# Optimization experiments

Measured on AMD Instinct MI355X. Metric: run time of the kernel, lower is better.

## Reference

```python
import jax, jax.numpy as jnp
import numpy as np

B, S, T, D, H = 2, 2048, 2048, 512, 8
HD = D // H
CLAMP = 1e9


def _padding_cross_mask(key):
    # emulate cross_mask(): valid prefixes for src and tgt sequences
    k1, k2 = jax.random.split(key)
    src_len = jax.random.randint(k1, (B,), S // 2, S + 1)  # [B]
    tgt_len = jax.random.randint(k2, (B,), T // 2, T + 1)  # [B]
    src_valid = jnp.arange(S)[None, :] < src_len[:, None]  # [B,S]
    tgt_valid = jnp.arange(T)[None, :] < tgt_len[:, None]  # [B,T]
    m = tgt_valid[:, :, None] & src_valid[:, None, :]      # [B,T,S]
    return m[:, None, :, :]                                 # [B,1,T,S]


def setup_inputs() -> dict:
    key = jax.random.key(0)
    ks = jax.random.split(key, 10)
    sc = 0.02
    return {
        "x": jax.random.normal(ks[0], (B, S, D), jnp.float32),
        "y": jax.random.normal(ks[1], (B, T, D), jnp.float32),
        "mask": _padding_cross_mask(ks[2]),
        "kv_w": jax.random.normal(ks[3], (D, 2 * D), jnp.float32) * sc,
        "kv_b": jax.random.normal(ks[4], (2 * D,), jnp.float32) * sc,
        "q_w": jax.random.normal(ks[5], (D, D), jnp.float32) * sc,
        "q_b": jax.random.normal(ks[6], (D,), jnp.float32) * sc,
        "o_w": jax.random.normal(ks[7], (D, D), jnp.float32) * sc,
        "o_b": jax.random.normal(ks[8], (D,), jnp.float32) * sc,
    }


def reference(x, y, mask, kv_w, kv_b, q_w, q_b, o_w, o_b):
    b, t, d = y.shape
    s = x.shape[1]
    kv = x @ kv_w + kv_b                               # [B,S,2D]
    q = y @ q_w + q_b                                  # [B,T,D]
    kv = kv.reshape(b, s, H, 2 * HD).transpose(0, 2, 1, 3)  # [B,H,S,2hd]
    q = q.reshape(b, t, H, HD).transpose(0, 2, 1, 3)        # [B,H,T,hd]
    k, v = kv[..., :HD], kv[..., HD:]
    scores = jnp.einsum("bhtd,bhsd->bhts", q, k) / jnp.sqrt(jnp.float32(HD))
    scores = jnp.where(mask, scores, -jnp.inf)
    scores = jnp.clip(scores, -CLAMP, CLAMP)
    attn = jax.nn.softmax(scores, axis=-1)             # [B,H,T,S]
    vals = jnp.einsum("bhts,bhsd->bhtd", attn, v)
    vals = vals.transpose(0, 2, 1, 3).reshape(b, t, d)
    return vals @ o_w + o_b
```

## Files before the change

### kernel.cpp

```cpp
#include <hip/hip_runtime.h>
#include <hip/hip_bf16.h>
#include <stdint.h>

#define BN 2
#define SL 2048
#define TL 2048
#define DD 512
#define HN 8
#define HDIM 64
#define NSPLIT 2
#define NCHUNK ((SL / NSPLIT) / 64)
#define QSCALE 0.1803368801111f
#define MFIX 12.0f

typedef __attribute__((ext_vector_type(8))) short bf16x8;
typedef __attribute__((ext_vector_type(4))) float f32x4;

static __device__ __forceinline__ unsigned short f2bf(float f) {
    union { float f; unsigned int u; } c; c.f = f;
    unsigned int u = c.u;
    unsigned int r = (u + 0x7fffu + ((u >> 16) & 1u)) >> 16;
    return (unsigned short)r;
}

static __device__ __forceinline__ void gload_lds16(const void* g, void* l) {
    __builtin_amdgcn_global_load_lds(
        (const __attribute__((address_space(1))) unsigned int*)g,
        (__attribute__((address_space(3))) unsigned int*)l, 16, 0, 0);
}

__global__ __launch_bounds__(256) void prep_kernel(
    const float* __restrict__ x, const float* __restrict__ y,
    const float* __restrict__ kv_w, const float* __restrict__ q_w,
    const float* __restrict__ o_w, const void* __restrict__ mask,
    unsigned short* __restrict__ xb, unsigned short* __restrict__ yb,
    unsigned short* __restrict__ kvwT, unsigned short* __restrict__ qwT,
    unsigned short* __restrict__ owT, int* __restrict__ lens,
    float* __restrict__ vmean)
{
    __shared__ unsigned short lds[64][80];
    __shared__ int kind_sh;
    __shared__ int lpart[4];
    int bx = blockIdx.x;
    int tid = threadIdx.x;
    if (bx < 2048) {
        const float* src = (bx < 1024) ? x : y;
        unsigned short* dst = (bx < 1024) ? xb : yb;
        long long i = ((long long)(bx & 1023) * 256 + tid) * 8;
        float4 v0 = *(const float4*)&src[i];
        float4 v1 = *(const float4*)&src[i + 4];
        unsigned long long p0 =
            (unsigned long long)f2bf(v0.x) | ((unsigned long long)f2bf(v0.y) << 16) |
            ((unsigned long long)f2bf(v0.z) << 32) | ((unsigned long long)f2bf(v0.w) << 48);
        unsigned long long p1 =
            (unsigned long long)f2bf(v1.x) | ((unsigned long long)f2bf(v1.y) << 16) |
            ((unsigned long long)f2bf(v1.z) << 32) | ((unsigned long long)f2bf(v1.w) << 48);
        *(unsigned long long*)&dst[i] = p0;
        *(unsigned long long*)&dst[i + 4] = p1;
        return;
    }
    if (bx >= 2308) {
        float4 z = {0.f, 0.f, 0.f, 0.f};
        ((float4*)vmean)[tid] = z;
        return;
    }
    if (bx >= 2304) {
        int blk = bx - 2304;
        int b = blk >> 1, is_tgt = blk & 1;
        if (tid == 0) {
            unsigned int v = *(const unsigned int*)mask;
            int kind = 0;
            if (v == 0x01010101u) kind = 1;
            else if (v == 0x3f800000u) kind = 2;
            else if (v == 0x3f803f80u) kind = 3;
            kind_sh = kind;
        }
        __syncthreads();
        int kind = kind_sh;
        int lane = tid & 63, wid = tid >> 6;
        int cnt = 0;
        for (int i = tid; i < (is_tgt ? TL : SL); i += 256) {
            long long idx = is_tgt ? ((long long)(b * TL + i)) * SL
                                   : ((long long)(b * TL + 0)) * SL + i;
            bool bit;
            if (kind == 0)      bit = ((const int*)mask)[idx] != 0;
            else if (kind == 1) bit = ((const unsigned char*)mask)[idx] != 0;
            else if (kind == 2) bit = ((const float*)mask)[idx] != 0.0f;
            else                bit = ((const unsigned short*)mask)[idx] != 0;
            cnt += bit ? 1 : 0;
        }
        #pragma unroll
        for (int off = 32; off >= 1; off >>= 1) cnt += __shfl_xor(cnt, off, 64);
        if (lane == 0) lpart[wid] = cnt;
        __syncthreads();
        if (tid == 0)
            lens[is_tgt * 2 + b] = lpart[0] + lpart[1] + lpart[2] + lpart[3];
        return;
    }
    const float* W; unsigned short* Wt; int N, tb;
    if (bx < 2176)      { W = kv_w; Wt = kvwT; N = 1024; tb = bx - 2048; }
    else if (bx < 2240) { W = q_w;  Wt = qwT;  N = 512;  tb = bx - 2176; }
    else                { W = o_w;  Wt = owT;  N = 512;  tb = bx - 2240; }
    int nblk = N / 64;
    int n0 = (tb % nblk) * 64, k0 = (tb / nblk) * 64;
    #pragma unroll
    for (int i = 0; i < 4; ++i) {
        int fi = tid + i * 256;
        int kl = fi >> 4;
        int nl = (fi & 15) * 4;
        float4 v = *(const float4*)&W[(long long)(k0 + kl) * N + n0 + nl];
        lds[nl + 0][kl] = f2bf(v.x);
        lds[nl + 1][kl] = f2bf(v.y);
        lds[nl + 2][kl] = f2bf(v.z);
        lds[nl + 3][kl] = f2bf(v.w);
    }
    __syncthreads();
    #pragma unroll
    for (int i = 0; i < 2; ++i) {
        int fi = tid + i * 256;
        int nl = fi >> 3;
        int kl = (fi & 7) * 8;
        *(bf16x8*)&Wt[(long long)(n0 + nl) * 512 + k0 + kl] = *(const bf16x8*)&lds[nl][kl];
    }
}

static __device__ __forceinline__ void mainloop_64x128(
    const unsigned short* __restrict__ Ab, const unsigned short* __restrict__ Bt,
    int m0, int n0, int tid,
    unsigned short* Alds,
    unsigned short* Blds,
    f32x4 (&acc)[2][4])
{
    int lane = tid & 63, wid = tid >> 6;
    int wr = wid >> 1, wc = wid & 1;
    int lr = lane & 15, lg = lane >> 4;
    int rl = lane >> 2;
    int sc = (lane & 3) ^ ((rl >> 1) & 3);

    auto stage = [&](int buf, int kt) {
        #pragma unroll
        for (int j = 0; j < 3; ++j) {
            int seg = wid * 3 + j;
            if (seg < 4) {
                int row = seg * 16 + rl;
                gload_lds16(&Ab[((long long)(m0 + row)) * 512 + kt * 32 + sc * 8],
                            (char*)(Alds + buf * 2048) + seg * 1024);
            } else {
                int s2 = seg - 4;
                int row = s2 * 16 + rl;
                gload_lds16(&Bt[((long long)(n0 + row)) * 512 + kt * 32 + sc * 8],
                            (char*)(Blds + buf * 4096) + s2 * 1024);
            }
        }
    };
    auto frag = [&](const unsigned short* base, int row) -> bf16x8 {
        int slot = lg ^ ((row >> 1) & 3);
        return *(const bf16x8*)((const char*)base + row * 64 + slot * 16);
    };

    stage(0, 0);
    stage(1, 1);
    for (int kt = 0; kt < 16; ++kt) {
        int buf = kt & 3;
        if (kt < 15) asm volatile("s_waitcnt vmcnt(3)" ::: "memory");
        else         asm volatile("s_waitcnt vmcnt(0)" ::: "memory");
        __builtin_amdgcn_s_barrier();
        __builtin_amdgcn_sched_barrier(0);
        if (kt + 2 < 16) stage((kt + 2) & 3, kt + 2);
        bf16x8 bfr[4];
        #pragma unroll
        for (int ni = 0; ni < 4; ++ni)
            bfr[ni] = frag(Blds + buf * 4096, wc * 64 + ni * 16 + lr);
        #pragma unroll
        for (int mi = 0; mi < 2; ++mi) {
            bf16x8 afr = frag(Alds + buf * 2048, wr * 32 + mi * 16 + lr);
            #pragma unroll
            for (int ni = 0; ni < 4; ++ni)
                acc[mi][ni] = __builtin_amdgcn_mfma_f32_16x16x32_bf16(
                                  afr, bfr[ni], acc[mi][ni], 0, 0, 0);
        }
    }
}

__global__ __launch_bounds__(256) void gemm_kvq(
    const unsigned short* __restrict__ xb, const unsigned short* __restrict__ yb,
    const unsigned short* __restrict__ kvwT, const unsigned short* __restrict__ qwT,
    const float* __restrict__ kv_b, const float* __restrict__ q_b,
    const int* __restrict__ lens,
    unsigned short* __restrict__ Kbuf, unsigned short* __restrict__ Vtbuf,
    unsigned short* __restrict__ Qbuf, float* __restrict__ vmean)
{
    __shared__ __align__(16) unsigned short Alds[4][64 * 32];
    __shared__ __align__(16) unsigned short Blds[4][128 * 32];
    int gid = blockIdx.x;
    int swz = (gid & 7) * 96 + (gid >> 3);
    int nidx = swz % 12;
    int m0 = (swz / 12) * 64;
    bool isq = nidx >= 8;
    if (isq && (m0 & 2047) >= lens[2 + (m0 >> 11)]) return;
    const unsigned short* Ab = isq ? yb : xb;
    const unsigned short* Bt = isq ? qwT : kvwT;
    const float* bias = isq ? q_b : kv_b;
    int n0 = (isq ? (nidx - 8) : nidx) * 128;
    int tid = threadIdx.x;
    int lane = tid & 63, wid = tid >> 6;
    int wr = wid >> 1, wc = wid & 1;
    int lr = lane & 15, lg = lane >> 4;

    f32x4 acc[2][4] = {};
    mainloop_64x128(Ab, Bt, m0, n0, tid, &Alds[0][0], &Blds[0][0], acc);

    float vsum[4] = {0.f, 0.f, 0.f, 0.f};
    #pragma unroll
    for (int mi = 0; mi < 2; ++mi)
    #pragma unroll
    for (int ni = 0; ni < 4; ++ni) {
        int n = n0 + wc * 64 + ni * 16 + lr;
        int mbase = m0 + wr * 32 + mi * 16 + lg * 4;
        float bv = bias[n];
        int b = mbase >> 11;
        int s = mbase & 2047;
        if (!isq) {
            int h = n >> 7, j = n & 127;
            if (j < HDIM) {
                long long base = (((long long)(b * HN + h)) * SL + s) * HDIM + j;
                #pragma unroll
                for (int r = 0; r < 4; ++r)
                    Kbuf[base + (long long)r * HDIM] = f2bf(acc[mi][ni][r] + bv);
            } else {
                int d = j - HDIM;
                long long base = (((long long)(b * HN + h)) * HDIM + d) * SL + s;
                unsigned long long p = 0;
                #pragma unroll
                for (int r = 0; r < 4; ++r)
                    p |= (unsigned long long)f2bf(acc[mi][ni][r] + bv) << (16 * r);
                *(unsigned long long*)&Vtbuf[base] = p;
                vsum[ni] += ((acc[mi][ni][0] + bv) + (acc[mi][ni][1] + bv)) +
                            ((acc[mi][ni][2] + bv) + (acc[mi][ni][3] + bv));
            }
        } else {
            int h = n >> 6, j = n & 63;
            long long base = (((long long)(b * HN + h)) * TL + s) * HDIM + j;
            #pragma unroll
            for (int r = 0; r < 4; ++r)
                Qbuf[base + (long long)r * HDIM] = f2bf((acc[mi][ni][r] + bv) * QSCALE);
        }
    }
    if (!isq && wc == 1) {
        int bh = (m0 >> 11) * HN + (n0 >> 7);
        #pragma unroll
        for (int ni = 0; ni < 4; ++ni) {
            float v = vsum[ni];
            v += __shfl_xor(v, 16, 64);
            v += __shfl_xor(v, 32, 64);
            if (lg == 0)
                atomicAdd(&vmean[bh * HDIM + ni * 16 + lr], v * (1.0f / SL));
        }
    }
}

__global__ __launch_bounds__(256) void gemm_out(
    const unsigned short* __restrict__ Ab, const unsigned short* __restrict__ Bt,
    const float* __restrict__ bias, float* __restrict__ outF)
{
    __shared__ __align__(16) unsigned short Alds[4][64 * 32];
    __shared__ __align__(16) unsigned short Blds[4][128 * 32];
    const int N = 512;
    int n0 = blockIdx.x * 128;
    int m0 = blockIdx.y * 64;
    int tid = threadIdx.x;
    int lane = tid & 63, wid = tid >> 6;
    int wr = wid >> 1, wc = wid & 1;
    int lr = lane & 15, lg = lane >> 4;

    f32x4 acc[2][4] = {};
    mainloop_64x128(Ab, Bt, m0, n0, tid, &Alds[0][0], &Blds[0][0], acc);

    #pragma unroll
    for (int mi = 0; mi < 2; ++mi)
    #pragma unroll
    for (int ni = 0; ni < 4; ++ni) {
        int n = n0 + wc * 64 + ni * 16 + lr;
        int mbase = m0 + wr * 32 + mi * 16 + lg * 4;
        float bv = bias[n];
        #pragma unroll
        for (int r = 0; r < 4; ++r)
            outF[(long long)(mbase + r) * N + n] = acc[mi][ni][r] + bv;
    }
}

__global__ __launch_bounds__(512) void attn_kernel(
    const unsigned short* __restrict__ Q,
    const unsigned short* __restrict__ K,
    const unsigned short* __restrict__ Vt,
    const int* __restrict__ lens,
    float* __restrict__ pml,
    float* __restrict__ pacc)
{
    __shared__ unsigned short Kt[2][4096];
    __shared__ unsigned short Vl[2][4096];
    __shared__ unsigned int P32[8][16][32];
    int idx = blockIdx.x;
    int gid = (idx & 7) * 64 + (idx >> 3);
    int t0 = (gid & 15) * 128;
    int bhsp = gid >> 4;
    int bh = bhsp >> 1;
    int sp = bhsp & 1;
    int b = bh >> 3;
    int tid = threadIdx.x;
    int lane = tid & 63, wid = tid >> 6;
    int tcol = lane & 15, lg = lane >> 4;
    int t0w = t0 + wid * 16;
    int src_len = lens[b];
    int tgt_len = lens[2 + b];
    if (t0 >= tgt_len) return;
    int sbase = sp * (SL / NSPLIT);

    int nch = (src_len - sbase + 63) >> 6;
    if (nch > NCHUNK) nch = NCHUNK;
    if (nch <= 0) {
        #pragma unroll
        for (int dc = 0; dc < 4; ++dc)
            #pragma unroll
            for (int r = 0; r < 4; ++r) {
                long long rowidx = (long long)bh * TL + t0w + lg * 4 + r;
                pacc[(rowidx * NSPLIT + sp) * 64 + dc * 16 + tcol] = 0.0f;
            }
        if (lg == 0) {
            long long rowidx = (long long)bh * TL + t0w + tcol;
            pml[rowidx * NSPLIT + sp] = 0.0f;
        }
        return;
    }

    const unsigned short* Qb = Q + ((long long)bh * TL) * HDIM;
    const unsigned short* Kb = K + ((long long)bh * SL) * HDIM;
    const unsigned short* Vb = Vt + ((long long)bh * HDIM) * SL;

    bf16x8 qf0 = *(const bf16x8*)&Qb[(t0w + tcol) * HDIM + lg * 8];
    bf16x8 qf1 = *(const bf16x8*)&Qb[(t0w + tcol) * HDIM + 32 + lg * 8];
    asm volatile("" : "+v"(qf0), "+v"(qf1));

    int sub = lane >> 3;
    int scol = (lane & 7) ^ sub;
    auto stage = [&](int buf, int s0) {
        int g = wid;
        int row = g * 8 + sub;
        gload_lds16(&Kb[(s0 + row) * HDIM + scol * 8],
                    (char*)&Kt[buf][0] + g * 1024);
        gload_lds16(&Vb[(long long)row * SL + s0 + scol * 8],
                    (char*)&Vl[buf][0] + g * 1024);
    };

    f32x4 accv[4] = {};
    float l_run = 0.0f;
    int pswz = (tcol & 7) << 2;

    stage(0, sbase);

    for (int sc2 = 0; sc2 < nch; ++sc2) {
        int s0 = sbase + sc2 * 64;
        asm volatile("s_waitcnt vmcnt(0)" ::: "memory");
        __syncthreads();
        if (sc2 + 1 < nch) stage((sc2 + 1) & 1, s0 + 64);
        const char* Kl = (const char*)&Kt[sc2 & 1][0];
        const char* Vlb = (const char*)&Vl[sc2 & 1][0];

        float sv[4][4];
        __builtin_amdgcn_s_setprio(1);
        #pragma unroll
        for (int st = 0; st < 4; ++st) {
            int krow = st * 16 + tcol;
            int swz = (krow & 7) << 4;
            bf16x8 kf0 = *(const bf16x8*)(Kl + krow * 128 + ((lg << 4) ^ swz));
            bf16x8 kf1 = *(const bf16x8*)(Kl + krow * 128 + (((lg + 4) << 4) ^ swz));
            f32x4 sa = {};
            sa = __builtin_amdgcn_mfma_f32_16x16x32_bf16(kf0, qf0, sa, 0, 0, 0);
            sa = __builtin_amdgcn_mfma_f32_16x16x32_bf16(kf1, qf1, sa, 0, 0, 0);
            #pragma unroll
            for (int r = 0; r < 4; ++r) sv[st][r] = sa[r];
        }
        __builtin_amdgcn_s_setprio(0);
        if (s0 + 64 > src_len) {
            #pragma unroll
            for (int st = 0; st < 4; ++st)
                #pragma unroll
                for (int r = 0; r < 4; ++r) {
                    int s = s0 + st * 16 + lg * 4 + r;
                    if (s >= src_len) sv[st][r] = -1e30f;
                }
        }
        float ps[4];
        #pragma unroll
        for (int st = 0; st < 4; ++st) {
            float p0 = __builtin_amdgcn_exp2f(sv[st][0] - MFIX);
            float p1 = __builtin_amdgcn_exp2f(sv[st][1] - MFIX);
            float p2 = __builtin_amdgcn_exp2f(sv[st][2] - MFIX);
            float p3 = __builtin_amdgcn_exp2f(sv[st][3] - MFIX);
            ps[st] = (p0 + p1) + (p2 + p3);
            unsigned int w0, w1;
            asm("v_cvt_pk_bf16_f32 %0, %1, %2" : "=v"(w0) : "v"(p0), "v"(p1));
            asm("v_cvt_pk_bf16_f32 %0, %1, %2" : "=v"(w1) : "v"(p2), "v"(p3));
            int wsw = (st * 8 + lg * 2) ^ pswz;
            *(unsigned long long*)&P32[wid][tcol][wsw] =
                (unsigned long long)w0 | ((unsigned long long)w1 << 32);
        }
        float psum = (ps[0] + ps[1]) + (ps[2] + ps[3]);
        psum += __shfl_xor(psum, 16, 64);
        psum += __shfl_xor(psum, 32, 64);
        l_run += psum;
        asm volatile("s_waitcnt lgkmcnt(0)" ::: "memory");
        __builtin_amdgcn_sched_barrier(0);
        __builtin_amdgcn_s_setprio(1);
        #pragma unroll
        for (int c = 0; c < 2; ++c) {
            bf16x8 pf = *(const bf16x8*)&P32[wid][tcol][(c * 16 + lg * 4) ^ pswz];
            #pragma unroll
            for (int dc = 0; dc < 4; ++dc) {
                int vrow = dc * 16 + tcol;
                bf16x8 vf = *(const bf16x8*)(Vlb + vrow * 128 +
                                             ((((c * 4 + lg) << 4)) ^ ((vrow & 7) << 4)));
                accv[dc] = __builtin_amdgcn_mfma_f32_16x16x32_bf16(pf, vf, accv[dc], 0, 0, 0);
            }
        }
        __builtin_amdgcn_s_setprio(0);
    }

    #pragma unroll
    for (int dc = 0; dc < 4; ++dc)
        #pragma unroll
        for (int r = 0; r < 4; ++r) {
            long long rowidx = (long long)bh * TL + t0w + lg * 4 + r;
            pacc[(rowidx * NSPLIT + sp) * 64 + dc * 16 + tcol] = accv[dc][r];
        }
    if (lg == 0) {
        long long rowidx = (long long)bh * TL + t0w + tcol;
        pml[rowidx * NSPLIT + sp] = l_run;
    }
}

__global__ __launch_bounds__(256) void combine_kernel(
    const float* __restrict__ pml, const float* __restrict__ pacc,
    const float* __restrict__ vmean, const int* __restrict__ lens,
    unsigned short* __restrict__ valsb)
{
    int lane = threadIdx.x & 63, wid = threadIdx.x >> 6;
    const int rows_total = BN * HN * TL;
    for (int row = blockIdx.x * 4 + wid; row < rows_total; row += gridDim.x * 4) {
        int bh = row >> 11, t = row & 2047;
        int b = bh >> 3, h = bh & 7;
        float o;
        if (t >= lens[2 + b]) {
            o = vmean[bh * HDIM + lane];
        } else {
            float l = pml[row * 2 + 0] + pml[row * 2 + 1];
            float a1 = pacc[((long long)row * 2 + 0) * 64 + lane];
            float a2 = pacc[((long long)row * 2 + 1) * 64 + lane];
            o = (a1 + a2) / l;
        }
        valsb[((long long)(b * TL + t)) * DD + h * HDIM + lane] = f2bf(o);
    }
}

extern "C" void kernel_launch(void* const* d_in, const int* in_sizes, int n_in,
                              void* d_out, int out_size, void* d_ws, size_t ws_size,
                              hipStream_t stream)
{
    const float* x    = (const float*)d_in[0];
    const float* y    = (const float*)d_in[1];
    const void*  mask = d_in[2];
    const float* kv_w = (const float*)d_in[3];
    const float* kv_b = (const float*)d_in[4];
    const float* q_w  = (const float*)d_in[5];
    const float* q_b  = (const float*)d_in[6];
    const float* o_w  = (const float*)d_in[7];
    const float* o_b  = (const float*)d_in[8];
    float* out = (float*)d_out;

    char* ws = (char*)d_ws;
    int* lens = (int*)ws;
    unsigned short* Qbuf  = (unsigned short*)(ws + 256);
    unsigned short* Kbuf  = Qbuf + (size_t)2097152;
    unsigned short* Vtbuf = Kbuf + (size_t)2097152;
    float* pml  = (float*)(Vtbuf + (size_t)2097152);
    float* pacc = pml + (size_t)262144;
    unsigned short* valsb = (unsigned short*)(pacc + (size_t)4194304);
    unsigned short* kvwT = valsb + (size_t)2097152;
    unsigned short* qwT  = kvwT + (size_t)524288;
    unsigned short* owT  = qwT + (size_t)262144;
    float* vmean = (float*)(owT + (size_t)262144);
    unsigned short* xb = (unsigned short*)pacc;
    unsigned short* yb = xb + (size_t)2097152;

    prep_kernel<<<2309, 256, 0, stream>>>(x, y, kv_w, q_w, o_w, mask,
                                          xb, yb, kvwT, qwT, owT, lens, vmean);
    gemm_kvq<<<768, 256, 0, stream>>>(xb, yb, kvwT, qwT, kv_b, q_b,
                                      lens, Kbuf, Vtbuf, Qbuf, vmean);
    attn_kernel<<<512, 512, 0, stream>>>(Qbuf, Kbuf, Vtbuf, lens, pml, pacc);
    combine_kernel<<<2048, 256, 0, stream>>>(pml, pacc, vmean, lens, valsb);
    gemm_out<<<dim3(4, 64), 256, 0, stream>>>(valsb, owT, o_b, out);
}
```

Before: 70.00 us.

## Interleave source chunks across splits and deepen K/V prefetch to four buffers

Changes the split-K partitioning so each of the two splits takes alternating 64-wide source chunks instead of contiguous halves. This balances work when the source length is ragged and removes the empty-split early-exit path. It also moves from double to quad buffering with a prefetch distance of two, using a partial vmcnt wait and a raw s_barrier. The trade-off is double the K/V shared memory, which may lower occupancy.

Result: no change. 70.24 us (+0.3%).

```diff
diff --git a/kernel.cpp b/kernel.cpp
--- a/kernel.cpp
+++ b/kernel.cpp
@@ -9,7 +9,6 @@
 #define HN 8
 #define HDIM 64
 #define NSPLIT 2
-#define NCHUNK ((SL / NSPLIT) / 64)
 #define QSCALE 0.1803368801111f
 #define MFIX 12.0f
 
@@ -297,8 +296,8 @@
     float* __restrict__ pml,
     float* __restrict__ pacc)
 {
-    __shared__ unsigned short Kt[2][4096];
-    __shared__ unsigned short Vl[2][4096];
+    __shared__ unsigned short Kt[4][4096];
+    __shared__ unsigned short Vl[4][4096];
     __shared__ unsigned int P32[8][16][32];
     int idx = blockIdx.x;
     int gid = (idx & 7) * 64 + (idx >> 3);
@@ -314,24 +313,10 @@
     int src_len = lens[b];
     int tgt_len = lens[2 + b];
     if (t0 >= tgt_len) return;
-    int sbase = sp * (SL / NSPLIT);
-
-    int nch = (src_len - sbase + 63) >> 6;
-    if (nch > NCHUNK) nch = NCHUNK;
-    if (nch <= 0) {
-        #pragma unroll
-        for (int dc = 0; dc < 4; ++dc)
-            #pragma unroll
-            for (int r = 0; r < 4; ++r) {
-                long long rowidx = (long long)bh * TL + t0w + lg * 4 + r;
-                pacc[(rowidx * NSPLIT + sp) * 64 + dc * 16 + tcol] = 0.0f;
-            }
-        if (lg == 0) {
-            long long rowidx = (long long)bh * TL + t0w + tcol;
-            pml[rowidx * NSPLIT + sp] = 0.0f;
-        }
-        return;
-    }
+
+    int nsch = (src_len + 63) >> 6;
+    if (nsch > SL / 64) nsch = SL / 64;
+    int nch = (nsch - sp + 1) >> 1;
 
     const unsigned short* Qb = Q + ((long long)bh * TL) * HDIM;
     const unsigned short* Kb = K + ((long long)bh * SL) * HDIM;
@@ -356,15 +341,18 @@
     float l_run = 0.0f;
     int pswz = (tcol & 7) << 2;
 
-    stage(0, sbase);
-
-    for (int sc2 = 0; sc2 < nch; ++sc2) {
-        int s0 = sbase + sc2 * 64;
-        asm volatile("s_waitcnt vmcnt(0)" ::: "memory");
-        __syncthreads();
-        if (sc2 + 1 < nch) stage((sc2 + 1) & 1, s0 + 64);
-        const char* Kl = (const char*)&Kt[sc2 & 1][0];
-        const char* Vlb = (const char*)&Vl[sc2 & 1][0];
+    stage(0, sp * 64);
+    if (nch > 1) stage(1, (2 + sp) * 64);
+
+    for (int c = 0; c < nch; ++c) {
+        int s0 = (2 * c + sp) * 64;
+        if (c + 1 < nch) asm volatile("s_waitcnt vmcnt(2)" ::: "memory");
+        else             asm volatile("s_waitcnt vmcnt(0)" ::: "memory");
+        __builtin_amdgcn_s_barrier();
+        __builtin_amdgcn_sched_barrier(0);
+        if (c + 2 < nch) stage((c + 2) & 3, (2 * (c + 2) + sp) * 64);
+        const char* Kl = (const char*)&Kt[c & 3][0];
+        const char* Vlb = (const char*)&Vl[c & 3][0];
 
         float sv[4][4];
         __builtin_amdgcn_s_setprio(1);
@@ -413,13 +401,13 @@
         __builtin_amdgcn_sched_barrier(0);
         __builtin_amdgcn_s_setprio(1);
         #pragma unroll
-        for (int c = 0; c < 2; ++c) {
-            bf16x8 pf = *(const bf16x8*)&P32[wid][tcol][(c * 16 + lg * 4) ^ pswz];
+        for (int c2 = 0; c2 < 2; ++c2) {
+            bf16x8 pf = *(const bf16x8*)&P32[wid][tcol][(c2 * 16 + lg * 4) ^ pswz];
             #pragma unroll
             for (int dc = 0; dc < 4; ++dc) {
                 int vrow = dc * 16 + tcol;
                 bf16x8 vf = *(const bf16x8*)(Vlb + vrow * 128 +
-                                             ((((c * 4 + lg) << 4)) ^ ((vrow & 7) << 4)));
+                                             ((((c2 * 4 + lg) << 4)) ^ ((vrow & 7) << 4)));
                 accv[dc] = __builtin_amdgcn_mfma_f32_16x16x32_bf16(pf, vf, accv[dc], 0, 0, 0);
             }
         }
```
